# Optimization experiments

Hardware: AMD Instinct MI355X
Metric: run time of the kernel (lower is better)

The kernel has to match this reference:

```python
import jax, jax.numpy as jnp
import numpy as np

EMBED_DIM = 512
N_HEADS = 8
HEAD_DIM = EMBED_DIM // N_HEADS
MAX_H = 64
MAX_W = 48
B, H, W = 2, 64, 48


def setup_inputs() -> dict:
    key = jax.random.key(0)
    k1, k2, k3, k4, k5 = jax.random.split(key, 5)
    x = jax.random.normal(k1, (B, H, W, EMBED_DIM), dtype=jnp.float32)
    # Linear weights stored as [in, out] (torch stores [out, in]; math is x @ W_in_out)
    w_qkv = jax.random.normal(k2, (EMBED_DIM, 3 * EMBED_DIM), dtype=jnp.float32) * (EMBED_DIM ** -0.5)
    w_out = jax.random.normal(k3, (EMBED_DIM, EMBED_DIM), dtype=jnp.float32) * (EMBED_DIM ** -0.5)
    rel_row_tab = jax.random.normal(k4, (2 * MAX_H - 1, N_HEADS), dtype=jnp.float32) * 0.02
    rel_col_tab = jax.random.normal(k5, (2 * MAX_W - 1, N_HEADS), dtype=jnp.float32) * 0.02
    return {"x": x, "w_qkv": w_qkv, "w_out": w_out,
            "rel_row_tab": rel_row_tab, "rel_col_tab": rel_col_tab}


def _rel_bias(rel_row_tab, rel_col_tab, height, width):
    # 2D relative position bias: [n_heads, S, S]
    row_idx = jnp.repeat(jnp.arange(height), width)          # [S]
    col_idx = jnp.tile(jnp.arange(width), height)            # [S]
    rel_row = jnp.clip(row_idx[:, None] - row_idx[None, :] + MAX_H - 1, 0, 2 * MAX_H - 2)
    rel_col = jnp.clip(col_idx[:, None] - col_idx[None, :] + MAX_W - 1, 0, 2 * MAX_W - 2)
    bias = rel_row_tab[rel_row] + rel_col_tab[rel_col]       # [S, S, n_heads]
    return jnp.transpose(bias, (2, 0, 1))                    # [n_heads, S, S]


def reference(x, w_qkv, w_out, rel_row_tab, rel_col_tab):
    b, h, w, d = x.shape
    s = h * w
    x_flat = x.reshape(b, s, d)
    qkv = x_flat @ w_qkv                                     # [b, s, 3d]
    qkv = qkv.reshape(b, s, 3, N_HEADS, HEAD_DIM)
    qkv = jnp.transpose(qkv, (2, 0, 3, 1, 4))                # [3, b, nh, s, hd]
    q, k, v = qkv[0], qkv[1], qkv[2]
    scale = HEAD_DIM ** -0.5
    attn = jnp.einsum('bhqd,bhkd->bhqk', q, k) * scale       # [b, nh, s, s]
    attn = attn + _rel_bias(rel_row_tab, rel_col_tab, h, w)[None]
    attn = jax.nn.softmax(attn, axis=-1)
    out = jnp.einsum('bhqk,bhkd->bhqd', attn, v)             # [b, nh, s, hd]
    out = jnp.transpose(out, (0, 2, 1, 3)).reshape(b, s, d)
    out = out @ w_out
    return out.reshape(b, h, w, d)
```

## Files before the change

kernel.cpp:

```cpp
#include <hip/hip_runtime.h>
#include <hip/hip_bf16.h>

#define S_TOK 3072
#define NHEADS 8

typedef __attribute__((ext_vector_type(8))) short short8;
typedef __attribute__((ext_vector_type(4))) float floatx4;
typedef __attribute__((ext_vector_type(4))) unsigned short ushortx4;

__device__ __forceinline__ unsigned short f2bf(float f) {
  union { float f; unsigned u; } v; v.f = f;
  unsigned r = v.u + 0x7fffu + ((v.u >> 16) & 1u);
  return (unsigned short)(r >> 16);
}
__device__ __forceinline__ float bf2f(unsigned short h) {
  union { unsigned u; float f; } v; v.u = (unsigned)h << 16;
  return v.f;
}
__device__ __forceinline__ unsigned pack2bf(float a, float b) {
  __hip_bfloat162 h = __float22bfloat162_rn(make_float2(a, b));
  union { __hip_bfloat162 h; unsigned u; } c; c.h = h;
  return c.u;
}
__device__ __forceinline__ void gload16(const void* g, void* l) {
  __builtin_amdgcn_global_load_lds(
      (const __attribute__((address_space(1))) unsigned int*)g,
      (__attribute__((address_space(3))) unsigned int*)l, 16, 0, 0);
}

__global__ __launch_bounds__(256) void ga_conv_all(
    const float* __restrict__ X, const float* __restrict__ Wq,
    const float* __restrict__ Wo, unsigned short* __restrict__ xh,
    unsigned short* __restrict__ xl, unsigned short* __restrict__ wqh,
    unsigned short* __restrict__ wql, unsigned short* __restrict__ woh,
    unsigned short* __restrict__ wol) {
  const int blk = blockIdx.x;
  const int t = threadIdx.x;
  if (blk < 1536) {
    const int c = blk * 256 + t;
    const int m = c >> 6;
    const int c8 = (c & 63) << 3;
    const float* src = X + (size_t)m * 512 + c8;
    float4 v0 = *(const float4*)src, v1 = *(const float4*)(src + 4);
    float vv[8] = {v0.x, v0.y, v0.z, v0.w, v1.x, v1.y, v1.z, v1.w};
    union { unsigned short s[8]; short8 v; } hh, ll;
#pragma unroll
    for (int e = 0; e < 8; ++e) {
      hh.s[e] = f2bf(vv[e]);
      ll.s[e] = f2bf(vv[e] - bf2f(hh.s[e]));
    }
    const size_t dst = (size_t)m * 512 + (c8 ^ ((m & 7) << 3));
    *(short8*)&xh[dst] = hh.v;
    *(short8*)&xl[dst] = ll.v;
    return;
  }
  const int wq = (blk < 1728);
  const int b2 = wq ? (blk - 1536) : (blk - 1728);
  const int N = wq ? 1536 : 512;
  const float* W = wq ? Wq : Wo;
  unsigned short* th = wq ? wqh : woh;
  unsigned short* tl = wq ? wql : wol;
  const int k0 = (b2 & 7) * 64, n0 = (b2 >> 3) * 64;
  __shared__ float Ts[64][65];
#pragma unroll
  for (int i = 0; i < 4; ++i) {
    const int r = (t >> 4) + i * 16, c4 = (t & 15) * 4;
    float4 v = *(const float4*)&W[(size_t)(k0 + r) * N + n0 + c4];
    Ts[r][c4] = v.x; Ts[r][c4 + 1] = v.y; Ts[r][c4 + 2] = v.z; Ts[r][c4 + 3] = v.w;
  }
  __syncthreads();
#pragma unroll
  for (int j = 0; j < 2; ++j) {
    const int chunk = t * 2 + j;
    const int nl = chunk >> 3, m8 = chunk & 7;
    const int n = n0 + nl;
    const int ks = (m8 * 8) ^ ((n & 7) << 3);
    union { unsigned short s[8]; short8 v; } hh, ll;
#pragma unroll
    for (int e = 0; e < 8; ++e) {
      float f = Ts[ks + e][nl];
      hh.s[e] = f2bf(f);
      ll.s[e] = f2bf(f - bf2f(hh.s[e]));
    }
    const size_t dst = (size_t)n * 512 + k0 + m8 * 8;
    *(short8*)&th[dst] = hh.v;
    *(short8*)&tl[dst] = ll.v;
  }
}

template <int BM, int BN>
__global__ __launch_bounds__(256, 2) void ga_mm3(
    const unsigned short* __restrict__ Ah, const unsigned short* __restrict__ Al,
    const unsigned short* __restrict__ Bh, const unsigned short* __restrict__ Bl,
    unsigned short* __restrict__ Qd, unsigned short* __restrict__ Kd,
    unsigned short* __restrict__ Vd) {
  const int tid = threadIdx.x;
  const int w = tid >> 6, l = tid & 63;
  const int g = l >> 4, ln = l & 15;
  const int wm = w >> 1, wn = w & 1;
  const int m0 = blockIdx.x * BM;
  const int n0 = blockIdx.y * BN;
  constexpr int MI = BM / 32;
  constexpr int NI = BN / 32;
  __shared__ unsigned short Alds[2][BM * 64];
  __shared__ unsigned short Blds[2][BN * 64];
  floatx4 acc[MI][NI];
#pragma unroll
  for (int mi = 0; mi < MI; ++mi)
#pragma unroll
    for (int ni = 0; ni < NI; ++ni)
#pragma unroll
      for (int r = 0; r < 4; ++r) acc[mi][ni][r] = 0.f;

  for (int k0 = 0; k0 < 512; k0 += 64) {
    __syncthreads();
    {
      constexpr int PWA = (BM * 128) / 4096;
      constexpr int PWB = (BN * 128) / 4096;
      const char* ga_h = (const char*)(Ah + (size_t)m0 * 512 + k0);
      const char* ga_l = (const char*)(Al + (size_t)m0 * 512 + k0);
      const char* gb_h = (const char*)(Bh + (size_t)n0 * 512 + k0);
      const char* gb_l = (const char*)(Bl + (size_t)n0 * 512 + k0);
#pragma unroll
      for (int i = 0; i < PWA; ++i) {
        const int off = (w * PWA + i) * 1024;
        const int gb = ((off >> 7) + (l >> 3)) * 1024 + (l & 7) * 16;
        gload16(ga_h + gb, (char*)&Alds[0][0] + off);
        gload16(ga_l + gb, (char*)&Alds[1][0] + off);
      }
#pragma unroll
      for (int i = 0; i < PWB; ++i) {
        const int off = (w * PWB + i) * 1024;
        const int gb = ((off >> 7) + (l >> 3)) * 1024 + (l & 7) * 16;
        gload16(gb_h + gb, (char*)&Blds[0][0] + off);
        gload16(gb_l + gb, (char*)&Blds[1][0] + off);
      }
    }
    asm volatile("s_waitcnt vmcnt(0)" ::: "memory");
    __syncthreads();
#pragma unroll
    for (int kk = 0; kk < 64; kk += 32) {
      const int kbase = kk + g * 8;
      short8 ah[MI], al[MI], bh[NI], bl[NI];
#pragma unroll
      for (int mi = 0; mi < MI; ++mi) {
        const int row = wm * (BM / 2) + mi * 16 + ln;
        const int a = row * 64 + (kbase ^ ((row & 7) << 3));
        ah[mi] = *(const short8*)&Alds[0][a];
        al[mi] = *(const short8*)&Alds[1][a];
      }
#pragma unroll
      for (int ni = 0; ni < NI; ++ni) {
        const int row = wn * (BN / 2) + ni * 16 + ln;
        const int a = row * 64 + (kbase ^ ((row & 7) << 3));
        bh[ni] = *(const short8*)&Blds[0][a];
        bl[ni] = *(const short8*)&Blds[1][a];
      }
#pragma unroll
      for (int mi = 0; mi < MI; ++mi)
#pragma unroll
        for (int ni = 0; ni < NI; ++ni) {
          acc[mi][ni] = __builtin_amdgcn_mfma_f32_16x16x32_bf16(
              ah[mi], bh[ni], acc[mi][ni], 0, 0, 0);
          acc[mi][ni] = __builtin_amdgcn_mfma_f32_16x16x32_bf16(
              al[mi], bh[ni], acc[mi][ni], 0, 0, 0);
          acc[mi][ni] = __builtin_amdgcn_mfma_f32_16x16x32_bf16(
              ah[mi], bl[ni], acc[mi][ni], 0, 0, 0);
        }
    }
  }
  const int b = m0 / S_TOK;
  const int s_base = (m0 % S_TOK) + wm * (BM / 2);
#pragma unroll
  for (int ni = 0; ni < NI; ++ni) {
    const int ng = n0 + wn * (BN / 2) + ni * 16;
    const int which = ng >> 9;
    const int h = (ng >> 6) & 7;
    const int d = (ng & 63) + ln;
    unsigned short* hp = (which == 0 ? Qd : which == 1 ? Kd : Vd) +
                         (size_t)(b * 8 + h) * S_TOK * 64;
    const float qs = (which == 0) ? 0.18033688f : 1.0f;
#pragma unroll
    for (int mi = 0; mi < MI; ++mi)
#pragma unroll
      for (int r = 0; r < 4; ++r) {
        const int s = s_base + mi * 16 + g * 4 + r;
        const size_t idx =
            (size_t)s * 64 + ((which == 1) ? (d ^ ((s & 7) << 3)) : d);
        hp[idx] = f2bf(acc[mi][ni][r] * qs);
      }
  }
}

__global__ __launch_bounds__(256) void ga_vtrans(
    const unsigned short* __restrict__ V, unsigned short* __restrict__ Vt2) {
  const int t = threadIdx.x;
  const int tile = blockIdx.x;
  const int bh = blockIdx.y;
  __shared__ unsigned short Ts[96][72];
  const unsigned short* vp = V + ((size_t)bh * S_TOK + tile * 96) * 64;
#pragma unroll
  for (int it = 0; it < 3; ++it) {
    int c = it * 256 + t;
    int s = c >> 3, d8 = c & 7;
    short8 v = *(const short8*)&vp[(size_t)s * 64 + d8 * 8];
    *(short8*)&Ts[s][d8 * 8] = v;
  }
  __syncthreads();
  unsigned short* op = Vt2 + ((size_t)bh * 32 + tile) * 8192;
#pragma unroll
  for (int it = 0; it < 4; ++it) {
    int c2 = it * 256 + t;
    int a = c2 * 8;
    int d = a >> 7;
    int pos0 = (a & 127) ^ ((d & 7) << 3);
    short8 o;
    if (pos0 < 96) {
      const int base = (pos0 & 96) + ((pos0 >> 3) & 3) * 4;
#pragma unroll
      for (int j = 0; j < 8; ++j) {
        const int key = base + ((j >> 2) << 4) + (j & 3);
        o[j] = (short)Ts[key][d];
      }
    } else {
#pragma unroll
      for (int j = 0; j < 8; ++j) o[j] = 0;
    }
    *(short8*)&op[a] = o;
  }
}

__global__ __launch_bounds__(256) void ga_attn16(
    const unsigned short* __restrict__ Q, const unsigned short* __restrict__ Kg,
    const unsigned short* __restrict__ Vt2, const float* __restrict__ rowtab,
    const float* __restrict__ coltab, float* __restrict__ Opart,
    float* __restrict__ Lpart, int tiles_per_split) {
  const int tid = threadIdx.x;
  const int w = tid >> 6;
  const int l = tid & 63;
  const int g = l >> 4;
  const int ln = l & 15;
  const int bh = blockIdx.y;
  const int sp = blockIdx.z;
  const int h = bh & 7;
  const int q0 = blockIdx.x * 128 + w * 32;

  __shared__ float rtab[127];
  __shared__ float ctab[95];
  __shared__ unsigned short Klds[6144];
  __shared__ unsigned short Vlds[8192];
  for (int i = tid; i < 127; i += 256) rtab[i] = rowtab[i * 8 + h] * 1.44269504f;
  for (int i = tid; i < 95; i += 256) ctab[i] = coltab[i * 8 + h] * 1.44269504f;
  __syncthreads();

  const unsigned short* Qp = Q + (size_t)bh * S_TOK * 64;
  const unsigned short* Kp = Kg + (size_t)bh * S_TOK * 64;
  const unsigned short* Vp = Vt2 + (size_t)bh * 32 * 8192;

  int qr[2], qc[2];
  short8 qf[2][2];
  float ctr[2][3][4];
#pragma unroll
  for (int u = 0; u < 2; ++u) {
    const int q = q0 + u * 16 + ln;
    qr[u] = q / 48;
    qc[u] = q - qr[u] * 48;
    qf[u][0] = *(const short8*)&Qp[(size_t)q * 64 + g * 8];
    qf[u][1] = *(const short8*)&Qp[(size_t)q * 64 + 32 + g * 8];
    const float* cb = &ctab[qc[u] - g * 4 + 47];
#pragma unroll
    for (int m = 0; m < 3; ++m)
#pragma unroll
      for (int r = 0; r < 4; ++r) ctr[u][m][r] = cb[-(16 * m + r)];
  }

  short8 ones;
  {
    union { unsigned short s[8]; short8 v; } on;
#pragma unroll
    for (int j = 0; j < 8; ++j) on.s[j] = 0x3F80;
    ones = on.v;
  }

  floatx4 o_acc[2][4];
  floatx4 o5[2];
#pragma unroll
  for (int u = 0; u < 2; ++u) {
#pragma unroll
    for (int r = 0; r < 4; ++r) o5[u][r] = 0.f;
#pragma unroll
    for (int dt = 0; dt < 4; ++dt)
#pragma unroll
      for (int r = 0; r < 4; ++r) o_acc[u][dt][r] = 0.f;
  }

  const int t0 = sp * tiles_per_split;
  for (int t = t0; t < t0 + tiles_per_split; ++t) {
    __syncthreads();
    {
      const char* kg = (const char*)(Kp + (size_t)t * 96 * 64);
      const char* vg = (const char*)(Vp + (size_t)t * 8192);
#pragma unroll
      for (int i = 0; i < 3; ++i) {
        const int off = w * 3072 + i * 1024;
        gload16(kg + off + l * 16, (char*)Klds + off);
      }
#pragma unroll
      for (int i = 0; i < 4; ++i) {
        const int off = w * 4096 + i * 1024;
        gload16(vg + off + l * 16, (char*)Vlds + off);
      }
      asm volatile("s_waitcnt vmcnt(0)" ::: "memory");
      __syncthreads();
    }
    float rt[2][2];
#pragma unroll
    for (int u = 0; u < 2; ++u) {
      rt[u][0] = rtab[qr[u] + 63 - 2 * t] - 12.0f;
      rt[u][1] = rtab[qr[u] + 62 - 2 * t] - 12.0f;
    }
    const int swz = (ln & 7) << 3;
#pragma unroll
    for (int kc32 = 0; kc32 < 3; ++kc32) {
      float e[2][2][4];
#pragma unroll
      for (int kh = 0; kh < 2; ++kh) {
        const int kt = kc32 * 2 + kh;
        const int rb = (kt * 16 + ln) * 64;
        short8 kf0 = *(const short8*)&Klds[rb + ((g * 8) ^ swz)];
        short8 kf1 = *(const short8*)&Klds[rb + ((32 + g * 8) ^ swz)];
        const int m = kt % 3, wrap = kt / 3;
#pragma unroll
        for (int u = 0; u < 2; ++u) {
          floatx4 s = {0.f, 0.f, 0.f, 0.f};
          s = __builtin_amdgcn_mfma_f32_16x16x32_bf16(kf0, qf[u][0], s, 0, 0, 0);
          s = __builtin_amdgcn_mfma_f32_16x16x32_bf16(kf1, qf[u][1], s, 0, 0, 0);
          const float rtw = rt[u][wrap];
#pragma unroll
          for (int r = 0; r < 4; ++r)
            e[u][kh][r] = __builtin_amdgcn_exp2f(s[r] + rtw + ctr[u][m][r]);
        }
      }
      short8 pf[2];
#pragma unroll
      for (int u = 0; u < 2; ++u) {
        union { unsigned uu[4]; short8 v; } pk;
        pk.uu[0] = pack2bf(e[u][0][0], e[u][0][1]);
        pk.uu[1] = pack2bf(e[u][0][2], e[u][0][3]);
        pk.uu[2] = pack2bf(e[u][1][0], e[u][1][1]);
        pk.uu[3] = pack2bf(e[u][1][2], e[u][1][3]);
        pf[u] = pk.v;
      }
#pragma unroll
      for (int dt = 0; dt < 4; ++dt) {
        const int vrow = dt * 16 + ln;
        short8 vf = *(const short8*)&Vlds[vrow * 128 +
                                          ((kc32 * 32 + g * 8) ^ swz)];
        o_acc[0][dt] =
            __builtin_amdgcn_mfma_f32_16x16x32_bf16(pf[0], vf, o_acc[0][dt], 0, 0, 0);
        o_acc[1][dt] =
            __builtin_amdgcn_mfma_f32_16x16x32_bf16(pf[1], vf, o_acc[1][dt], 0, 0, 0);
      }
      o5[0] = __builtin_amdgcn_mfma_f32_16x16x32_bf16(pf[0], ones, o5[0], 0, 0, 0);
      o5[1] = __builtin_amdgcn_mfma_f32_16x16x32_bf16(pf[1], ones, o5[1], 0, 0, 0);
    }
  }
  const size_t rowbase = (size_t)(sp * 16 + bh) * S_TOK;
#pragma unroll
  for (int u = 0; u < 2; ++u) {
    if (ln == 0) {
#pragma unroll
      for (int r = 0; r < 4; ++r)
        Lpart[rowbase + q0 + u * 16 + g * 4 + r] = o5[u][r];
    }
#pragma unroll
    for (int dt = 0; dt < 4; ++dt)
#pragma unroll
      for (int r = 0; r < 4; ++r)
        Opart[(rowbase + q0 + u * 16 + g * 4 + r) * 64 + dt * 16 + ln] =
            o_acc[u][dt][r];
  }
}

template <int NS>
__global__ __launch_bounds__(256, 2) void ga_outmm(
    const float* __restrict__ Opart, const float* __restrict__ Lpart,
    const unsigned short* __restrict__ Bh_, float* __restrict__ Out) {
  const int tid = threadIdx.x;
  const int w = tid >> 6, l = tid & 63;
  const int g = l >> 4, ln = l & 15;
  const int wm = w >> 1, wn = w & 1;
  const int m0 = blockIdx.x * 64;
  const int n0 = blockIdx.y * 64;
  __shared__ unsigned short Alds[64 * 64];
  __shared__ unsigned short Blds[64 * 64];
  floatx4 acc[2][2];
#pragma unroll
  for (int mi = 0; mi < 2; ++mi)
#pragma unroll
    for (int ni = 0; ni < 2; ++ni)
#pragma unroll
      for (int r = 0; r < 4; ++r) acc[mi][ni][r] = 0.f;

  const int lm = tid >> 2, lk4 = tid & 3;
  const int m = m0 + lm;
  const int b = (m >= S_TOK) ? 1 : 0;
  const int q = m - b * S_TOK;

  for (int h = 0; h < 8; ++h) {
    __syncthreads();
    {
      const char* gb = (const char*)(Bh_ + (size_t)n0 * 512 + h * 64);
#pragma unroll
      for (int i = 0; i < 2; ++i) {
        const int off = (w * 2 + i) * 1024;
        const int gbo = ((off >> 7) + (l >> 3)) * 1024 + (l & 7) * 16;
        gload16(gb + gbo, (char*)Blds + off);
      }
    }
    {
      const int bh = b * 8 + h;
      float v[16];
      float ls = 0.f;
#pragma unroll
      for (int s = 0; s < NS; ++s) {
        const size_t row = (size_t)(s * 16 + bh) * S_TOK + q;
        ls += Lpart[row];
        const float* op = &Opart[row * 64 + lk4 * 16];
#pragma unroll
        for (int j = 0; j < 4; ++j) {
          float4 o = *(const float4*)(op + j * 4);
          if (s == 0) {
            v[j * 4] = o.x; v[j * 4 + 1] = o.y;
            v[j * 4 + 2] = o.z; v[j * 4 + 3] = o.w;
          } else {
            v[j * 4] += o.x; v[j * 4 + 1] += o.y;
            v[j * 4 + 2] += o.z; v[j * 4 + 3] += o.w;
          }
        }
      }
      const float inv = 1.0f / ls;
      unsigned pk[8];
#pragma unroll
      for (int j = 0; j < 8; ++j)
        pk[j] = pack2bf(v[2 * j] * inv, v[2 * j + 1] * inv);
      const int sw = (lm & 7) << 3;
      unsigned short* ab = &Alds[lm * 64];
#pragma unroll
      for (int j = 0; j < 4; ++j)
        *(uint2*)&ab[(lk4 * 16 + j * 4) ^ sw] = make_uint2(pk[2 * j], pk[2 * j + 1]);
    }
    asm volatile("s_waitcnt vmcnt(0)" ::: "memory");
    __syncthreads();
#pragma unroll
    for (int kk = 0; kk < 64; kk += 32) {
      const int kbase = kk + g * 8;
      short8 af[2], bf[2];
#pragma unroll
      for (int mi = 0; mi < 2; ++mi) {
        const int row = wm * 32 + mi * 16 + ln;
        af[mi] = *(const short8*)&Alds[row * 64 + (kbase ^ ((row & 7) << 3))];
      }
#pragma unroll
      for (int ni = 0; ni < 2; ++ni) {
        const int row = wn * 32 + ni * 16 + ln;
        bf[ni] = *(const short8*)&Blds[row * 64 + (kbase ^ ((row & 7) << 3))];
      }
#pragma unroll
      for (int mi = 0; mi < 2; ++mi)
#pragma unroll
        for (int ni = 0; ni < 2; ++ni)
          acc[mi][ni] = __builtin_amdgcn_mfma_f32_16x16x32_bf16(
              af[mi], bf[ni], acc[mi][ni], 0, 0, 0);
    }
  }
#pragma unroll
  for (int mi = 0; mi < 2; ++mi)
#pragma unroll
    for (int ni = 0; ni < 2; ++ni)
#pragma unroll
      for (int r = 0; r < 4; ++r)
        Out[(size_t)(m0 + wm * 32 + mi * 16 + g * 4 + r) * 512 + n0 +
            wn * 32 + ni * 16 + ln] = acc[mi][ni][r];
}

extern "C" void kernel_launch(void* const* d_in, const int* in_sizes, int n_in,
                              void* d_out, int out_size, void* d_ws,
                              size_t ws_size, hipStream_t stream) {
  const float* x = (const float*)d_in[0];
  const float* w_qkv = (const float*)d_in[1];
  const float* w_out = (const float*)d_in[2];
  const float* rrow = (const float*)d_in[3];
  const float* rcol = (const float*)d_in[4];
  float* out = (float*)d_out;

  unsigned short* ws16 = (unsigned short*)d_ws;
  unsigned short* xh = ws16;
  unsigned short* xl = xh + 3145728;
  unsigned short* wqh = xl + 3145728;
  unsigned short* wql = wqh + 786432;
  unsigned short* woh = wql + 786432;
  unsigned short* wol = woh + 262144;
  unsigned short* Qb = wol + 262144;
  unsigned short* Kb = Qb + 3145728;
  unsigned short* Vb = Kb + 3145728;
  unsigned short* Vt2 = Vb + 3145728;
  float* Opart = (float*)(Vt2 + 4194304);
  const size_t base_bytes = (size_t)22020096 * 2;
  const size_t per_split = (size_t)(3145728 + 49152) * 4;
  const int nsplit = (ws_size >= base_bytes + 2 * per_split) ? 2 : 1;
  float* Lpart = Opart + (size_t)nsplit * 3145728;

  ga_conv_all<<<1792, 256, 0, stream>>>(x, w_qkv, w_out, xh, xl, wqh, wql, woh,
                                        wol);
  ga_mm3<128, 128><<<dim3(48, 12), 256, 0, stream>>>(
      xh, xl, wqh, wql, Qb, Kb, Vb);
  ga_vtrans<<<dim3(32, 16), 256, 0, stream>>>(Vb, Vt2);
  ga_attn16<<<dim3(24, 16, nsplit), 256, 0, stream>>>(
      Qb, Kb, Vt2, rrow, rcol, Opart, Lpart, 32 / nsplit);
  if (nsplit == 2)
    ga_outmm<2><<<dim3(96, 8), 256, 0, stream>>>(Opart, Lpart, woh, out);
  else
    ga_outmm<1><<<dim3(96, 8), 256, 0, stream>>>(Opart, Lpart, woh, out);
}
```

Before: 131.1 us.

## Interleave K and V tiles and double-buffer KV loads in attention kernel

K and transposed V are stored interleaved per 96-key tile in one contiguous buffer. The V-transposed layout is compacted to a 104-element padded row instead of a 128-wide swizzled row. The attention kernel now prefetches the next KV tile into a second LDS buffer while computing on the current one, so global-to-LDS loads overlap with MFMA work instead of stalling each iteration. This doubles the LDS footprint, which may lower occupancy, and the padded stride replaces the XOR swizzle, which could add bank conflicts.

```diff
diff --git a/kernel.cpp b/kernel.cpp
--- a/kernel.cpp
+++ b/kernel.cpp
@@ -3,6 +3,7 @@
 
 #define S_TOK 3072
 #define NHEADS 8
+#define KVT 12800
 
 typedef __attribute__((ext_vector_type(8))) short short8;
 typedef __attribute__((ext_vector_type(4))) float floatx4;
@@ -92,7 +93,7 @@
 __global__ __launch_bounds__(256, 2) void ga_mm3(
     const unsigned short* __restrict__ Ah, const unsigned short* __restrict__ Al,
     const unsigned short* __restrict__ Bh, const unsigned short* __restrict__ Bl,
-    unsigned short* __restrict__ Qd, unsigned short* __restrict__ Kd,
+    unsigned short* __restrict__ Qd, unsigned short* __restrict__ KV,
     unsigned short* __restrict__ Vd) {
   const int tid = threadIdx.x;
   const int w = tid >> 6, l = tid & 63;
@@ -177,23 +178,36 @@
     const int which = ng >> 9;
     const int h = (ng >> 6) & 7;
     const int d = (ng & 63) + ln;
-    unsigned short* hp = (which == 0 ? Qd : which == 1 ? Kd : Vd) +
-                         (size_t)(b * 8 + h) * S_TOK * 64;
+    const int bh = b * 8 + h;
     const float qs = (which == 0) ? 0.18033688f : 1.0f;
-#pragma unroll
-    for (int mi = 0; mi < MI; ++mi)
-#pragma unroll
-      for (int r = 0; r < 4; ++r) {
-        const int s = s_base + mi * 16 + g * 4 + r;
-        const size_t idx =
-            (size_t)s * 64 + ((which == 1) ? (d ^ ((s & 7) << 3)) : d);
-        hp[idx] = f2bf(acc[mi][ni][r] * qs);
-      }
+    if (which == 1) {
+      unsigned short* kp = KV + (size_t)bh * 32 * KVT;
+#pragma unroll
+      for (int mi = 0; mi < MI; ++mi)
+#pragma unroll
+        for (int r = 0; r < 4; ++r) {
+          const int s = s_base + mi * 16 + g * 4 + r;
+          const int tile = s / 96;
+          const int r96 = s - tile * 96;
+          kp[tile * KVT + r96 * 64 + (d ^ ((s & 7) << 3))] =
+              f2bf(acc[mi][ni][r]);
+        }
+    } else {
+      unsigned short* hp =
+          (which == 0 ? Qd : Vd) + (size_t)bh * S_TOK * 64;
+#pragma unroll
+      for (int mi = 0; mi < MI; ++mi)
+#pragma unroll
+        for (int r = 0; r < 4; ++r) {
+          const int s = s_base + mi * 16 + g * 4 + r;
+          hp[(size_t)s * 64 + d] = f2bf(acc[mi][ni][r] * qs);
+        }
+    }
   }
 }
 
 __global__ __launch_bounds__(256) void ga_vtrans(
-    const unsigned short* __restrict__ V, unsigned short* __restrict__ Vt2) {
+    const unsigned short* __restrict__ V, unsigned short* __restrict__ KV) {
   const int t = threadIdx.x;
   const int tile = blockIdx.x;
   const int bh = blockIdx.y;
@@ -207,34 +221,36 @@
     *(short8*)&Ts[s][d8 * 8] = v;
   }
   __syncthreads();
-  unsigned short* op = Vt2 + ((size_t)bh * 32 + tile) * 8192;
+  unsigned short* op = KV + ((size_t)bh * 32 + tile) * KVT + 6144;
 #pragma unroll
   for (int it = 0; it < 4; ++it) {
     int c2 = it * 256 + t;
-    int a = c2 * 8;
-    int d = a >> 7;
-    int pos0 = (a & 127) ^ ((d & 7) << 3);
-    short8 o;
-    if (pos0 < 96) {
-      const int base = (pos0 & 96) + ((pos0 >> 3) & 3) * 4;
-#pragma unroll
-      for (int j = 0; j < 8; ++j) {
-        const int key = base + ((j >> 2) << 4) + (j & 3);
-        o[j] = (short)Ts[key][d];
-      }
-    } else {
-#pragma unroll
-      for (int j = 0; j < 8; ++j) o[j] = 0;
-    }
-    *(short8*)&op[a] = o;
+    if (c2 < 832) {
+      const int d = c2 / 13;
+      const int kc8 = (c2 - d * 13) * 8;
+      short8 o;
+      if (kc8 < 96) {
+#pragma unroll
+        for (int j = 0; j < 8; ++j) {
+          const int p = kc8 + j;
+          const int key =
+              (p >> 5) * 32 + ((p >> 2) & 1) * 16 + ((p >> 3) & 3) * 4 + (p & 3);
+          o[j] = (short)Ts[key][d];
+        }
+      } else {
+#pragma unroll
+        for (int j = 0; j < 8; ++j) o[j] = 0;
+      }
+      *(short8*)&op[d * 104 + kc8] = o;
+    }
   }
 }
 
 __global__ __launch_bounds__(256) void ga_attn16(
-    const unsigned short* __restrict__ Q, const unsigned short* __restrict__ Kg,
-    const unsigned short* __restrict__ Vt2, const float* __restrict__ rowtab,
-    const float* __restrict__ coltab, float* __restrict__ Opart,
-    float* __restrict__ Lpart, int tiles_per_split) {
+    const unsigned short* __restrict__ Q, const unsigned short* __restrict__ KVg,
+    const float* __restrict__ rowtab, const float* __restrict__ coltab,
+    float* __restrict__ Opart, float* __restrict__ Lpart,
+    int tiles_per_split) {
   const int tid = threadIdx.x;
   const int w = tid >> 6;
   const int l = tid & 63;
@@ -247,15 +263,28 @@
 
   __shared__ float rtab[127];
   __shared__ float ctab[95];
-  __shared__ unsigned short Klds[6144];
-  __shared__ unsigned short Vlds[8192];
+  __shared__ unsigned short KVlds[2][KVT];
   for (int i = tid; i < 127; i += 256) rtab[i] = rowtab[i * 8 + h] * 1.44269504f;
   for (int i = tid; i < 95; i += 256) ctab[i] = coltab[i * 8 + h] * 1.44269504f;
+
+  const unsigned short* Qp = Q + (size_t)bh * S_TOK * 64;
+  const unsigned short* KVp = KVg + (size_t)bh * 32 * KVT;
+
+  const int t0 = sp * tiles_per_split;
+  const int tend = t0 + tiles_per_split;
+
+  auto STAGE = [&](int b, int t) {
+    const char* src = (const char*)(KVp + (size_t)t * KVT);
+    char* dst = (char*)&KVlds[b][0];
+#pragma unroll
+    for (int i = 0; i < 6; ++i)
+      gload16(src + i * 4096 + tid * 16, dst + i * 4096 + tid * 16);
+    if (tid < 64) gload16(src + 24576 + tid * 16, dst + 24576 + tid * 16);
+  };
+
+  STAGE(0, t0);
+  asm volatile("s_waitcnt vmcnt(0)" ::: "memory");
   __syncthreads();
-
-  const unsigned short* Qp = Q + (size_t)bh * S_TOK * 64;
-  const unsigned short* Kp = Kg + (size_t)bh * S_TOK * 64;
-  const unsigned short* Vp = Vt2 + (size_t)bh * 32 * 8192;
 
   int qr[2], qc[2];
   short8 qf[2][2];
@@ -294,25 +323,11 @@
       for (int r = 0; r < 4; ++r) o_acc[u][dt][r] = 0.f;
   }
 
-  const int t0 = sp * tiles_per_split;
-  for (int t = t0; t < t0 + tiles_per_split; ++t) {
-    __syncthreads();
-    {
-      const char* kg = (const char*)(Kp + (size_t)t * 96 * 64);
-      const char* vg = (const char*)(Vp + (size_t)t * 8192);
-#pragma unroll
-      for (int i = 0; i < 3; ++i) {
-        const int off = w * 3072 + i * 1024;
-        gload16(kg + off + l * 16, (char*)Klds + off);
-      }
-#pragma unroll
-      for (int i = 0; i < 4; ++i) {
-        const int off = w * 4096 + i * 1024;
-        gload16(vg + off + l * 16, (char*)Vlds + off);
-      }
-      asm volatile("s_waitcnt vmcnt(0)" ::: "memory");
-      __syncthreads();
-    }
+  int cur = 0;
+  for (int t = t0; t < tend; ++t) {
+    if (t + 1 < tend) STAGE(cur ^ 1, t + 1);
+    const unsigned short* kb = &KVlds[cur][0];
+    const unsigned short* vb = &KVlds[cur][6144];
     float rt[2][2];
 #pragma unroll
     for (int u = 0; u < 2; ++u) {
@@ -327,8 +342,8 @@
       for (int kh = 0; kh < 2; ++kh) {
         const int kt = kc32 * 2 + kh;
         const int rb = (kt * 16 + ln) * 64;
-        short8 kf0 = *(const short8*)&Klds[rb + ((g * 8) ^ swz)];
-        short8 kf1 = *(const short8*)&Klds[rb + ((32 + g * 8) ^ swz)];
+        short8 kf0 = *(const short8*)&kb[rb + ((g * 8) ^ swz)];
+        short8 kf1 = *(const short8*)&kb[rb + ((32 + g * 8) ^ swz)];
         const int m = kt % 3, wrap = kt / 3;
 #pragma unroll
         for (int u = 0; u < 2; ++u) {
@@ -354,8 +369,7 @@
 #pragma unroll
       for (int dt = 0; dt < 4; ++dt) {
         const int vrow = dt * 16 + ln;
-        short8 vf = *(const short8*)&Vlds[vrow * 128 +
-                                          ((kc32 * 32 + g * 8) ^ swz)];
+        short8 vf = *(const short8*)&vb[vrow * 104 + kc32 * 32 + g * 8];
         o_acc[0][dt] =
             __builtin_amdgcn_mfma_f32_16x16x32_bf16(pf[0], vf, o_acc[0][dt], 0, 0, 0);
         o_acc[1][dt] =
@@ -364,6 +378,9 @@
       o5[0] = __builtin_amdgcn_mfma_f32_16x16x32_bf16(pf[0], ones, o5[0], 0, 0, 0);
       o5[1] = __builtin_amdgcn_mfma_f32_16x16x32_bf16(pf[1], ones, o5[1], 0, 0, 0);
     }
+    asm volatile("s_waitcnt vmcnt(0)" ::: "memory");
+    __syncthreads();
+    cur ^= 1;
   }
   const size_t rowbase = (size_t)(sp * 16 + bh) * S_TOK;
 #pragma unroll
@@ -502,11 +519,11 @@
   unsigned short* woh = wql + 786432;
   unsigned short* wol = woh + 262144;
   unsigned short* Qb = wol + 262144;
-  unsigned short* Kb = Qb + 3145728;
-  unsigned short* Vb = Kb + 3145728;
-  unsigned short* Vt2 = Vb + 3145728;
-  float* Opart = (float*)(Vt2 + 4194304);
-  const size_t base_bytes = (size_t)22020096 * 2;
+  unsigned short* Vb = Qb + 3145728;
+  unsigned short* KV = Vb + 3145728;
+  float* Opart = (float*)(KV + 6553600);
+  const size_t base_bytes =
+      ((size_t)3145728 * 4 + 786432 * 2 + 262144 * 2 + 6553600) * 2;
   const size_t per_split = (size_t)(3145728 + 49152) * 4;
   const int nsplit = (ws_size >= base_bytes + 2 * per_split) ? 2 : 1;
   float* Lpart = Opart + (size_t)nsplit * 3145728;
@@ -514,10 +531,10 @@
   ga_conv_all<<<1792, 256, 0, stream>>>(x, w_qkv, w_out, xh, xl, wqh, wql, woh,
                                         wol);
   ga_mm3<128, 128><<<dim3(48, 12), 256, 0, stream>>>(
-      xh, xl, wqh, wql, Qb, Kb, Vb);
-  ga_vtrans<<<dim3(32, 16), 256, 0, stream>>>(Vb, Vt2);
+      xh, xl, wqh, wql, Qb, KV, Vb);
+  ga_vtrans<<<dim3(32, 16), 256, 0, stream>>>(Vb, KV);
   ga_attn16<<<dim3(24, 16, nsplit), 256, 0, stream>>>(
-      Qb, Kb, Vt2, rrow, rcol, Opart, Lpart, 32 / nsplit);
+      Qb, KV, rrow, rcol, Opart, Lpart, 32 / nsplit);
   if (nsplit == 2)
     ga_outmm<2><<<dim3(96, 8), 256, 0, stream>>>(Opart, Lpart, woh, out);
   else
```

After: 126.1 us. 3.8% less time.
